# Performance work log

Measured on AMD Instinct MI355X. Metric: run time of the kernel, lower is better.

## Reference

```python
import jax, jax.numpy as jnp
import numpy as np

B, S, D, H = 2, 4096, 256, 8
P = 64               # proj_dim_l
R = S // P           # proj_dim_r = 64, P*R == S
DH = D // H          # head_dim = 32


def setup_inputs() -> dict:
    key = jax.random.key(0)
    kx, kl, kr, kv, ko = jax.random.split(key, 5)
    scale = 0.05  # stand-in for xavier-uniform scale
    x  = jax.random.normal(kx, (B, S, D), dtype=jnp.float32)
    Wl = jax.random.normal(kl, (D, P), dtype=jnp.float32) * scale
    Wr = jax.random.normal(kr, (D, R), dtype=jnp.float32) * scale
    Wv = jax.random.normal(kv, (D, D), dtype=jnp.float32) * scale
    Wo = jax.random.normal(ko, (D, D), dtype=jnp.float32) * scale
    return {"x": x, "Wl": Wl, "Wr": Wr, "Wv": Wv, "Wo": Wo}


def reference(x, Wl, Wr, Wv, Wo):
    b, s, d = x.shape
    # value projection + head split -> (b, H, S, DH). Dropout p=0 (eval) = identity.
    v = (x @ Wv).reshape(b, s, H, DH).transpose(0, 2, 1, 3)
    # factorized score: row n is vec(outer(l_n, r_n)) of length P*R == S
    l = x @ Wl                                   # (b, S, P)
    r = x @ Wr                                   # (b, S, R)
    attn = (l[:, :, :, None] * r[:, :, None, :]).reshape(b, s, s)  # (b, S, S)
    score = jax.nn.softmax(attn, axis=-1)        # (b, S, S)
    # shared score across heads, per-head value matmul
    o = jnp.einsum('bnm,bhmd->bhnd', score, v)   # (b, H, S, DH)
    o = o.transpose(0, 2, 1, 3).reshape(b, s, d) # concat heads
    return o @ Wo
```

## Files before the change

### kernel.cpp

```cpp
#include <hip/hip_runtime.h>
#include <hip/hip_bf16.h>

typedef __attribute__((ext_vector_type(8))) __bf16 bf16x8;
typedef __attribute__((ext_vector_type(4))) __bf16 bf16x4;
typedef __attribute__((ext_vector_type(4))) float  f32x4;

#define MFMA16(a, b, c) __builtin_amdgcn_mfma_f32_16x16x32_bf16((a), (b), (c), 0, 0, 0)

static constexpr size_t OFF_WVT  = 0;
static constexpr size_t OFF_WLT  = OFF_WVT + 256 * 256 * 2;
static constexpr size_t OFF_WRT  = OFF_WLT + 64 * 256 * 2;
static constexpr size_t OFF_VT   = 1u << 20;
static constexpr size_t OFF_L    = 6u << 20;
static constexpr size_t OFF_R    = 8u << 20;
static constexpr size_t OFF_PART = 10u << 20;
static constexpr size_t OFF_ZP   = 26u << 20;

__device__ __forceinline__ float fast_exp2(float x) {
  float e;
  asm("v_exp_f32 %0, %1" : "=v"(e) : "v"(x));
  return e;
}

__device__ __forceinline__ bf16x8 cvt8(float4 a, float4 b) {
  bf16x8 o;
  o[0] = (__bf16)a.x; o[1] = (__bf16)a.y; o[2] = (__bf16)a.z; o[3] = (__bf16)a.w;
  o[4] = (__bf16)b.x; o[5] = (__bf16)b.y; o[6] = (__bf16)b.z; o[7] = (__bf16)b.w;
  return o;
}

__device__ __forceinline__ void gll16(const __bf16* g, __bf16* l) {
  __builtin_amdgcn_global_load_lds((const __attribute__((address_space(1))) void*)g,
                                   (__attribute__((address_space(3))) void*)l,
                                   16, 0, 0);
}

__global__ __launch_bounds__(256) void k_prepw(const float* __restrict__ Wv,
                                               const float* __restrict__ Wl,
                                               const float* __restrict__ Wr,
                                               const float* __restrict__ Wo,
                                               __bf16* __restrict__ Wvt,
                                               __bf16* __restrict__ Wlt,
                                               __bf16* __restrict__ Wrt) {
  const int blk = blockIdx.x;
  const int t = threadIdx.x;
  if (blk < 128) {
    const int idx = blk * 256 + t;
    if (idx < 16384) {
      const int k = idx >> 6, n = idx & 63;
      Wlt[n * 256 + k] = (__bf16)Wl[idx];
    } else {
      const int j = idx - 16384;
      const int k = j >> 6, n = j & 63;
      Wrt[n * 256 + k] = (__bf16)Wr[j];
    }
  } else {
    const int k = blk - 128;
    const int n = t;
    const float* wvr = Wv + (size_t)k * 256;
    float a0 = 0.f, a1 = 0.f, a2 = 0.f, a3 = 0.f;
#pragma unroll 4
    for (int j = 0; j < 256; j += 4) {
      a0 += wvr[j + 0] * Wo[(size_t)(j + 0) * 256 + n];
      a1 += wvr[j + 1] * Wo[(size_t)(j + 1) * 256 + n];
      a2 += wvr[j + 2] * Wo[(size_t)(j + 2) * 256 + n];
      a3 += wvr[j + 3] * Wo[(size_t)(j + 3) * 256 + n];
    }
    Wvt[(size_t)n * 256 + k] = (__bf16)((a0 + a1) + (a2 + a3));
  }
}

__global__ __launch_bounds__(256) void k_proj(const float* __restrict__ x,
                                              const __bf16* __restrict__ Wvt,
                                              const __bf16* __restrict__ Wlt,
                                              const __bf16* __restrict__ Wrt,
                                              __bf16* __restrict__ Vt,
                                              float* __restrict__ lbuf,
                                              float* __restrict__ rbuf) {
  __shared__ __align__(16) __bf16 vs[8 * 64 * 8];
  const int t = threadIdx.x;
  const int lane = t & 63, wave = t >> 6;
  const int l16 = lane & 15, quad = lane >> 4;
  const int wr = wave >> 1, wc = wave & 1;
  const int bid = blockIdx.x;
  const int q   = bid / 48;
  const int rmd = bid - q * 48;
  const int ct  = rmd >> 3;
  const int rbk = q * 8 + (rmd & 7);
  const __bf16* Wt;
  int colbase;
  if (ct < 4)       { Wt = Wvt; colbase = ct * 64; }
  else if (ct == 4) { Wt = Wlt; colbase = 0; }
  else              { Wt = Wrt; colbase = 0; }
  const int row0 = rbk * 64 + wr * 32;
  const int c0   = colbase + wc * 32;
  f32x4 acc[2][2] = {};
  for (int kk = 0; kk < 256; kk += 32) {
    const int ko = kk + quad * 8;
    const float* xr0 = x + (size_t)(row0 + l16) * 256 + ko;
    const float* xr1 = x + (size_t)(row0 + 16 + l16) * 256 + ko;
    bf16x8 a0 = cvt8(*(const float4*)xr0, *(const float4*)(xr0 + 4));
    bf16x8 a1 = cvt8(*(const float4*)xr1, *(const float4*)(xr1 + 4));
    bf16x8 b0 = *(const bf16x8*)(Wt + (size_t)(c0 + l16) * 256 + ko);
    bf16x8 b1 = *(const bf16x8*)(Wt + (size_t)(c0 + 16 + l16) * 256 + ko);
    acc[0][0] = MFMA16(a0, b0, acc[0][0]);
    acc[0][1] = MFMA16(a0, b1, acc[0][1]);
    acc[1][0] = MFMA16(a1, b0, acc[1][0]);
    acc[1][1] = MFMA16(a1, b1, acc[1][1]);
  }
  if (ct < 4) {
#pragma unroll
    for (int mt = 0; mt < 2; ++mt)
#pragma unroll
      for (int nt = 0; nt < 2; ++nt) {
        const int m8 = wr * 4 + mt * 2 + (quad >> 1);
        const int d  = wc * 32 + nt * 16 + l16;
        bf16x4 o;
        o.x = (__bf16)acc[mt][nt][0];
        o.y = (__bf16)acc[mt][nt][1];
        o.z = (__bf16)acc[mt][nt][2];
        o.w = (__bf16)acc[mt][nt][3];
        *(bf16x4*)(&vs[m8 * 512 + d * 8 + (quad & 1) * 4]) = o;
      }
    __syncthreads();
    const int m8 = t >> 5, s32 = t & 31;
    const int bat = rbk >> 6, mc = rbk & 63;
    bf16x8 a = *(const bf16x8*)(&vs[m8 * 512 + s32 * 16]);
    bf16x8 b = *(const bf16x8*)(&vs[m8 * 512 + s32 * 16 + 8]);
    __bf16* dst = Vt + (size_t)bat * 1048576 + (size_t)mc * 16384 +
                  m8 * 2048 + ct * 512 + s32 * 16;
    *(bf16x8*)dst       = a;
    *(bf16x8*)(dst + 8) = b;
  } else {
    float* dstb = (ct == 4) ? lbuf : rbuf;
#pragma unroll
    for (int mt = 0; mt < 2; ++mt)
#pragma unroll
      for (int nt = 0; nt < 2; ++nt) {
        const int col = c0 + nt * 16 + l16;
        const int gr  = rbk * 64 + wr * 32 + mt * 16 + quad * 4;
#pragma unroll
        for (int rr = 0; rr < 4; ++rr)
          dstb[(size_t)(gr + rr) * 64 + col] = acc[mt][nt][rr];
      }
  }
}

__global__ __launch_bounds__(256, 2) void k_attn(const float* __restrict__ lbuf,
                                                 const float* __restrict__ rbuf,
                                                 const __bf16* __restrict__ Vt,
                                                 __bf16* __restrict__ part,
                                                 float* __restrict__ zpart) {
  __shared__ __align__(16) char smem[69888];
  __bf16* vt0 = (__bf16*)smem;
  __bf16* vt1 = (__bf16*)(smem + 32768);
  float*  ls  = (float*)(smem + 65536);
  const int t = threadIdx.x;
  const int lane = t & 63, w = t >> 6;
  const int l16 = lane & 15, quad = lane >> 4;
  const int wr = w >> 1, wc = w & 1;
  const int bid = blockIdx.x;
  const int cmb = bid & 7;
  const int sp  = cmb >> 1;
  const int bat = cmb & 1;
  const int rbl = bid >> 3;
  const int g0  = bat * 4096 + rbl * 64;
  const __bf16* Vbase = Vt + (size_t)bat * 1048576;
  const int ck0 = sp * 16;

  {
    const int row = t >> 2, c = (t & 3) * 4;
    f32x4 v = *(const f32x4*)(lbuf + (size_t)(g0 + row) * 64 + ck0 + c);
    ls[row * 17 + c + 0] = v[0];
    ls[row * 17 + c + 1] = v[1];
    ls[row * 17 + c + 2] = v[2];
    ls[row * 17 + c + 3] = v[3];
  }
  const float LOG2E = 1.44269504088896f;
  float rreg[2][16];
#pragma unroll
  for (int mt = 0; mt < 2; ++mt) {
    const float* rp = rbuf + (size_t)(g0 + wr * 32 + mt * 16 + l16) * 64;
    f32x4 a = *(const f32x4*)(rp + quad * 8);
    f32x4 b = *(const f32x4*)(rp + quad * 8 + 4);
    f32x4 c = *(const f32x4*)(rp + 32 + quad * 8);
    f32x4 d = *(const f32x4*)(rp + 32 + quad * 8 + 4);
#pragma unroll
    for (int j = 0; j < 4; ++j) {
      rreg[mt][j]      = a[j] * LOG2E;
      rreg[mt][4 + j]  = b[j] * LOG2E;
      rreg[mt][8 + j]  = c[j] * LOG2E;
      rreg[mt][12 + j] = d[j] * LOG2E;
    }
  }

  f32x4 acc[2][8] = {};
  float zacc[2][2] = {{0.f, 0.f}, {0.f, 0.f}};

#define STAGE(KC, DST)                                                          \
  {                                                                             \
    const __bf16* src = Vbase + (size_t)(ck0 + (KC)) * 16384;                   \
    _Pragma("unroll")                                                           \
    for (int i = 0; i < 8; ++i)                                                 \
      gll16(src + (size_t)(i * 256 + t) * 8, (DST) + (i * 256 + (w << 6)) * 8); \
  }

#define AF_COMPUTE(KC, AF)                                                    \
  {                                                                           \
    _Pragma("unroll")                                                         \
    for (int mt = 0; mt < 2; ++mt) {                                          \
      const float lv = ls[(wr * 32 + mt * 16 + l16) * 17 + (KC)];             \
      _Pragma("unroll")                                                       \
      for (int kk = 0; kk < 2; ++kk)                                          \
        _Pragma("unroll")                                                     \
        for (int j = 0; j < 8; ++j) {                                         \
          const float e = fast_exp2(lv * rreg[mt][kk * 8 + j]);               \
          zacc[mt][kk] += e;                                                  \
          AF[mt][kk][j] = (__bf16)e;                                          \
        }                                                                     \
    }                                                                         \
  }

#define MFMA_PHASE(CUR, AF)                                                   \
  {                                                                           \
    _Pragma("unroll")                                                         \
    for (int kk = 0; kk < 2; ++kk)                                            \
      _Pragma("unroll")                                                       \
      for (int nt = 0; nt < 8; ++nt) {                                        \
        bf16x8 bv = *(const bf16x8*)((CUR) + (kk * 4 + quad) * 2048 +         \
                                     (wc * 128 + nt * 16 + l16) * 8);         \
        acc[0][nt] = MFMA16(AF[0][kk], bv, acc[0][nt]);                       \
        acc[1][nt] = MFMA16(AF[1][kk], bv, acc[1][nt]);                       \
      }                                                                       \
  }

  STAGE(0, vt0);
  __syncthreads();
  bf16x8 afA[2][2], afB[2][2];
  AF_COMPUTE(0, afA);

  for (int kc = 0; kc < 16; kc += 2) {
    STAGE(kc + 1, vt1);
    AF_COMPUTE(kc + 1, afB);
    MFMA_PHASE(vt0, afA);
    __syncthreads();
    if (kc + 2 < 16) {
      STAGE(kc + 2, vt0);
      AF_COMPUTE(kc + 2, afA);
    }
    MFMA_PHASE(vt1, afB);
    __syncthreads();
  }

#undef STAGE
#undef AF_COMPUTE
#undef MFMA_PHASE

#pragma unroll
  for (int mt = 0; mt < 2; ++mt) {
    float z = zacc[mt][0] + zacc[mt][1];
    z += __shfl_xor(z, 16);
    z += __shfl_xor(z, 32);
    if (wc == 0 && quad == 0)
      zpart[(size_t)sp * 8192 + g0 + wr * 32 + mt * 16 + l16] = z;
  }

  __bf16* ctile = (__bf16*)smem;
#pragma unroll
  for (int mt = 0; mt < 2; ++mt)
#pragma unroll
    for (int nt = 0; nt < 8; ++nt) {
      const int r0 = wr * 32 + mt * 16 + quad * 4;
      const int c  = wc * 128 + nt * 16 + l16;
#pragma unroll
      for (int rr = 0; rr < 4; ++rr)
        ctile[(r0 + rr) * 264 + c] = (__bf16)acc[mt][nt][rr];
    }
  __syncthreads();
  __bf16* pb = part + (size_t)sp * (8192 * 256);
#pragma unroll
  for (int p = 0; p < 8; ++p) {
    const int u = p * 256 + t;
    const int row = u >> 5, seg = u & 31;
    *(bf16x8*)(pb + (size_t)(g0 + row) * 256 + seg * 8) =
        *(const bf16x8*)(ctile + row * 264 + seg * 8);
  }
}

__global__ __launch_bounds__(256) void k_fix(const __bf16* __restrict__ part,
                                             const float* __restrict__ zpart,
                                             float* __restrict__ out) {
  const int idx = blockIdx.x * 256 + threadIdx.x;
  const int g = idx >> 5, seg = idx & 31;
  float z = 0.f;
#pragma unroll
  for (int s = 0; s < 4; ++s) z += zpart[(size_t)s * 8192 + g];
  const float iz = 1.0f / z;
  float sum[8] = {};
#pragma unroll
  for (int s = 0; s < 4; ++s) {
    bf16x8 p = *(const bf16x8*)(part + (size_t)s * (8192 * 256) + (size_t)g * 256 + seg * 8);
#pragma unroll
    for (int j = 0; j < 8; ++j) sum[j] += (float)p[j];
  }
  f32x4 o0, o1;
#pragma unroll
  for (int j = 0; j < 4; ++j) { o0[j] = sum[j] * iz; o1[j] = sum[4 + j] * iz; }
  float* dst = out + (size_t)g * 256 + seg * 8;
  *(f32x4*)dst       = o0;
  *(f32x4*)(dst + 4) = o1;
}

extern "C" void kernel_launch(void* const* d_in, const int* in_sizes, int n_in,
                              void* d_out, int out_size, void* d_ws, size_t ws_size,
                              hipStream_t stream) {
  const float* x  = (const float*)d_in[0];
  const float* Wl = (const float*)d_in[1];
  const float* Wr = (const float*)d_in[2];
  const float* Wv = (const float*)d_in[3];
  const float* Wo = (const float*)d_in[4];
  char* ws = (char*)d_ws;
  __bf16* Wvt = (__bf16*)(ws + OFF_WVT);
  __bf16* Wlt = (__bf16*)(ws + OFF_WLT);
  __bf16* Wrt = (__bf16*)(ws + OFF_WRT);
  __bf16* Vt  = (__bf16*)(ws + OFF_VT);
  float*  lb  = (float*)(ws + OFF_L);
  float*  rbf = (float*)(ws + OFF_R);
  __bf16* prt = (__bf16*)(ws + OFF_PART);
  float*  zp  = (float*)(ws + OFF_ZP);
  float*  out = (float*)d_out;

  k_prepw<<<384, 256, 0, stream>>>(Wv, Wl, Wr, Wo, Wvt, Wlt, Wrt);
  k_proj<<<768, 256, 0, stream>>>(x, Wvt, Wlt, Wrt, Vt, lb, rbf);
  k_attn<<<512, 256, 0, stream>>>(lb, rbf, Vt, prt, zp);
  k_fix<<<1024, 256, 0, stream>>>(prt, zp, out);
}
```

Before: 122.6 us.

## Deepen attention V staging to four half-size buffers with explicit vmcnt waits

The attention kernel now stages V in 8 KB-per-thread-group chunks across four LDS buffers, keeping three loads in flight. It replaces __syncthreads with explicit s_waitcnt vmcnt plus raw barriers and sched_barriers, so global-to-LDS loads overlap the exp and MFMA work. The number of steps doubles, each doing half the MFMAs, which adds barrier overhead per unit of work. Separately, the weight-fold prep kernel splits each 256-long dot product across four thread groups in a 1024-thread block and reduces the partial sums through shared memory, giving more parallelism to a small kernel.

```diff
diff --git a/kernel.cpp b/kernel.cpp
--- a/kernel.cpp
+++ b/kernel.cpp
@@ -35,17 +35,18 @@
                                    16, 0, 0);
 }
 
-__global__ __launch_bounds__(256) void k_prepw(const float* __restrict__ Wv,
-                                               const float* __restrict__ Wl,
-                                               const float* __restrict__ Wr,
-                                               const float* __restrict__ Wo,
-                                               __bf16* __restrict__ Wvt,
-                                               __bf16* __restrict__ Wlt,
-                                               __bf16* __restrict__ Wrt) {
+__global__ __launch_bounds__(1024) void k_prepw(const float* __restrict__ Wv,
+                                                const float* __restrict__ Wl,
+                                                const float* __restrict__ Wr,
+                                                const float* __restrict__ Wo,
+                                                __bf16* __restrict__ Wvt,
+                                                __bf16* __restrict__ Wlt,
+                                                __bf16* __restrict__ Wrt) {
+  __shared__ float red[3][256];
   const int blk = blockIdx.x;
   const int t = threadIdx.x;
-  if (blk < 128) {
-    const int idx = blk * 256 + t;
+  if (blk < 32) {
+    const int idx = blk * 1024 + t;
     if (idx < 16384) {
       const int k = idx >> 6, n = idx & 63;
       Wlt[n * 256 + k] = (__bf16)Wl[idx];
@@ -55,18 +56,24 @@
       Wrt[n * 256 + k] = (__bf16)Wr[j];
     }
   } else {
-    const int k = blk - 128;
-    const int n = t;
-    const float* wvr = Wv + (size_t)k * 256;
+    const int k  = blk - 32;
+    const int n  = t & 255;
+    const int jq = t >> 8;
+    const float* wvr = Wv + (size_t)k * 256 + jq * 64;
+    const float* wor = Wo + (size_t)(jq * 64) * 256 + n;
     float a0 = 0.f, a1 = 0.f, a2 = 0.f, a3 = 0.f;
 #pragma unroll 4
-    for (int j = 0; j < 256; j += 4) {
-      a0 += wvr[j + 0] * Wo[(size_t)(j + 0) * 256 + n];
-      a1 += wvr[j + 1] * Wo[(size_t)(j + 1) * 256 + n];
-      a2 += wvr[j + 2] * Wo[(size_t)(j + 2) * 256 + n];
-      a3 += wvr[j + 3] * Wo[(size_t)(j + 3) * 256 + n];
+    for (int j = 0; j < 64; j += 4) {
+      a0 += wvr[j + 0] * wor[(size_t)(j + 0) * 256];
+      a1 += wvr[j + 1] * wor[(size_t)(j + 1) * 256];
+      a2 += wvr[j + 2] * wor[(size_t)(j + 2) * 256];
+      a3 += wvr[j + 3] * wor[(size_t)(j + 3) * 256];
     }
-    Wvt[(size_t)n * 256 + k] = (__bf16)((a0 + a1) + (a2 + a3));
+    const float s = (a0 + a1) + (a2 + a3);
+    if (jq > 0) red[jq - 1][n] = s;
+    __syncthreads();
+    if (jq == 0)
+      Wvt[(size_t)n * 256 + k] = (__bf16)(s + red[0][n] + red[1][n] + red[2][n]);
   }
 }
 
@@ -152,8 +159,10 @@
                                                  __bf16* __restrict__ part,
                                                  float* __restrict__ zpart) {
   __shared__ __align__(16) char smem[69888];
-  __bf16* vt0 = (__bf16*)smem;
-  __bf16* vt1 = (__bf16*)(smem + 32768);
+  __bf16* vb0 = (__bf16*)smem;
+  __bf16* vb1 = (__bf16*)(smem + 16384);
+  __bf16* vb2 = (__bf16*)(smem + 32768);
+  __bf16* vb3 = (__bf16*)(smem + 49152);
   float*  ls  = (float*)(smem + 65536);
   const int t = threadIdx.x;
   const int lane = t & 63, w = t >> 6;
@@ -166,11 +175,11 @@
   const int rbl = bid >> 3;
   const int g0  = bat * 4096 + rbl * 64;
   const __bf16* Vbase = Vt + (size_t)bat * 1048576;
-  const int ck0 = sp * 16;
+  const int ck0 = sp * 32;
 
   {
     const int row = t >> 2, c = (t & 3) * 4;
-    f32x4 v = *(const f32x4*)(lbuf + (size_t)(g0 + row) * 64 + ck0 + c);
+    f32x4 v = *(const f32x4*)(lbuf + (size_t)(g0 + row) * 64 + sp * 16 + c);
     ls[row * 17 + c + 0] = v[0];
     ls[row * 17 + c + 1] = v[1];
     ls[row * 17 + c + 2] = v[2];
@@ -199,62 +208,84 @@
 
 #define STAGE(KC, DST)                                                          \
   {                                                                             \
-    const __bf16* src = Vbase + (size_t)(ck0 + (KC)) * 16384;                   \
+    const __bf16* src = Vbase + (size_t)(ck0 + (KC)) * 8192;                    \
     _Pragma("unroll")                                                           \
-    for (int i = 0; i < 8; ++i)                                                 \
+    for (int i = 0; i < 4; ++i)                                                 \
       gll16(src + (size_t)(i * 256 + t) * 8, (DST) + (i * 256 + (w << 6)) * 8); \
   }
 
-#define AF_COMPUTE(KC, AF)                                                    \
+#define AF_COMPUTE(KC)                                                        \
+  {                                                                           \
+    const int c16 = (KC) >> 1, hf = ((KC) & 1) * 8;                           \
+    _Pragma("unroll")                                                         \
+    for (int mt = 0; mt < 2; ++mt) {                                          \
+      const float lv = ls[(wr * 32 + mt * 16 + l16) * 17 + c16];              \
+      _Pragma("unroll")                                                       \
+      for (int j = 0; j < 8; ++j) {                                           \
+        const float e = fast_exp2(lv * rreg[mt][hf + j]);                     \
+        zacc[mt][(KC) & 1] += e;                                              \
+        af[mt][j] = (__bf16)e;                                                \
+      }                                                                       \
+    }                                                                         \
+  }
+
+#define MFMA_PHASE(CUR)                                                       \
   {                                                                           \
     _Pragma("unroll")                                                         \
-    for (int mt = 0; mt < 2; ++mt) {                                          \
-      const float lv = ls[(wr * 32 + mt * 16 + l16) * 17 + (KC)];             \
-      _Pragma("unroll")                                                       \
-      for (int kk = 0; kk < 2; ++kk)                                          \
-        _Pragma("unroll")                                                     \
-        for (int j = 0; j < 8; ++j) {                                         \
-          const float e = fast_exp2(lv * rreg[mt][kk * 8 + j]);               \
-          zacc[mt][kk] += e;                                                  \
-          AF[mt][kk][j] = (__bf16)e;                                          \
-        }                                                                     \
+    for (int nt = 0; nt < 8; ++nt) {                                          \
+      bf16x8 bv = *(const bf16x8*)((CUR) + quad * 2048 +                      \
+                                   (wc * 128 + nt * 16 + l16) * 8);           \
+      acc[0][nt] = MFMA16(af[0], bv, acc[0][nt]);                             \
+      acc[1][nt] = MFMA16(af[1], bv, acc[1][nt]);                             \
     }                                                                         \
   }
 
-#define MFMA_PHASE(CUR, AF)                                                   \
+#define STEP(CC, BCUR, SC, BST, VM)                                           \
   {                                                                           \
-    _Pragma("unroll")                                                         \
-    for (int kk = 0; kk < 2; ++kk)                                            \
-      _Pragma("unroll")                                                       \
-      for (int nt = 0; nt < 8; ++nt) {                                        \
-        bf16x8 bv = *(const bf16x8*)((CUR) + (kk * 4 + quad) * 2048 +         \
-                                     (wc * 128 + nt * 16 + l16) * 8);         \
-        acc[0][nt] = MFMA16(AF[0][kk], bv, acc[0][nt]);                       \
-        acc[1][nt] = MFMA16(AF[1][kk], bv, acc[1][nt]);                       \
-      }                                                                       \
-  }
-
-  STAGE(0, vt0);
+    STAGE(SC, BST);                                                           \
+    bf16x8 af[2];                                                             \
+    AF_COMPUTE(CC);                                                           \
+    asm volatile("s_waitcnt vmcnt(" #VM ")" ::: "memory");                    \
+    __builtin_amdgcn_s_barrier();                                             \
+    __builtin_amdgcn_sched_barrier(0);                                        \
+    MFMA_PHASE(BCUR);                                                         \
+    __builtin_amdgcn_s_barrier();                                             \
+    __builtin_amdgcn_sched_barrier(0);                                        \
+  }
+
+#define STEPX(CC, BCUR, VM)                                                   \
+  {                                                                           \
+    bf16x8 af[2];                                                             \
+    AF_COMPUTE(CC);                                                           \
+    asm volatile("s_waitcnt vmcnt(" #VM ")" ::: "memory");                    \
+    __builtin_amdgcn_s_barrier();                                             \
+    __builtin_amdgcn_sched_barrier(0);                                        \
+    MFMA_PHASE(BCUR);                                                         \
+    __builtin_amdgcn_s_barrier();                                             \
+    __builtin_amdgcn_sched_barrier(0);                                        \
+  }
+
+  STAGE(0, vb0);
+  STAGE(1, vb1);
+  STAGE(2, vb2);
   __syncthreads();
-  bf16x8 afA[2][2], afB[2][2];
-  AF_COMPUTE(0, afA);
-
-  for (int kc = 0; kc < 16; kc += 2) {
-    STAGE(kc + 1, vt1);
-    AF_COMPUTE(kc + 1, afB);
-    MFMA_PHASE(vt0, afA);
-    __syncthreads();
-    if (kc + 2 < 16) {
-      STAGE(kc + 2, vt0);
-      AF_COMPUTE(kc + 2, afA);
-    }
-    MFMA_PHASE(vt1, afB);
-    __syncthreads();
-  }
+
+  for (int c = 0; c < 28; c += 4) {
+    STEP(c + 0, vb0, c + 3, vb3, 12);
+    STEP(c + 1, vb1, c + 4, vb0, 12);
+    STEP(c + 2, vb2, c + 5, vb1, 12);
+    STEP(c + 3, vb3, c + 6, vb2, 12);
+  }
+  STEP (28, vb0, 31, vb3, 12);
+  STEPX(29, vb1, 8);
+  STEPX(30, vb2, 4);
+  STEPX(31, vb3, 0);
 
 #undef STAGE
 #undef AF_COMPUTE
 #undef MFMA_PHASE
+#undef STEP
+#undef STEPX
 
 #pragma unroll
   for (int mt = 0; mt < 2; ++mt) {
@@ -265,6 +296,7 @@
       zpart[(size_t)sp * 8192 + g0 + wr * 32 + mt * 16 + l16] = z;
   }
 
+  __syncthreads();
   __bf16* ctile = (__bf16*)smem;
 #pragma unroll
   for (int mt = 0; mt < 2; ++mt)
@@ -330,7 +362,7 @@
   float*  zp  = (float*)(ws + OFF_ZP);
   float*  out = (float*)d_out;
 
-  k_prepw<<<384, 256, 0, stream>>>(Wv, Wl, Wr, Wo, Wvt, Wlt, Wrt);
+  k_prepw<<<288, 1024, 0, stream>>>(Wv, Wl, Wr, Wo, Wvt, Wlt, Wrt);
   k_proj<<<768, 256, 0, stream>>>(x, Wvt, Wlt, Wrt, Vt, lb, rbf);
   k_attn<<<512, 256, 0, stream>>>(lb, rbf, Vt, prt, zp);
   k_fix<<<1024, 256, 0, stream>>>(prt, zp, out);
```

New measurement: 121.0 us. No clear change (-1.3%).
